# Kernel optimization log

Measured on AMD Instinct MI355X. Metric: run time of the kernel, lower is better.

## Reference

```python
import jax, jax.numpy as jnp
import numpy as np

EPS = 1e-12  # torch F.normalize default eps


def _l2norm(x):
    n = jnp.sqrt(jnp.sum(x * x, axis=-1, keepdims=True))
    return x / jnp.maximum(n, EPS)


def setup_inputs() -> dict:
    key = jax.random.key(0)
    ks = jax.random.split(key, 8)
    B, T, V = 4, 2048, 512
    C, H, NB = 512, 4, 64
    return {
        "x": jax.random.normal(ks[0], (B, T, V), dtype=jnp.float32),
        "basis": jax.random.normal(ks[1], (V, 2 * NB), dtype=jnp.float32),
        "shared_q_w": jax.random.normal(ks[2], (V, C), dtype=jnp.float32) * 0.02,
        "shared_k_w": jax.random.normal(ks[3], (V, C), dtype=jnp.float32) * 0.02,
        "v_coeffs": jax.random.normal(ks[4], (C, 2 * NB), dtype=jnp.float32) * 0.02,
        "o_coeffs": jax.random.normal(ks[5], (C, 2 * NB), dtype=jnp.float32) * 0.02,
        "decay_logits": jnp.linspace(1.0, 5.0, H, dtype=jnp.float32),
        "out_scale": jnp.float32(0.1),
    }


def reference(x, basis, shared_q_w, shared_k_w, v_coeffs, o_coeffs, decay_logits, out_scale):
    B, T, V = x.shape
    H = decay_logits.shape[0]
    C = shared_q_w.shape[1]
    D = C // H

    v_w = basis @ v_coeffs.T  # [V, C]
    o_w = basis @ o_coeffs.T  # [V, C]

    q = _l2norm(x @ shared_q_w)  # [B, T, C]
    k = _l2norm(x @ shared_k_w)
    v = x @ v_w

    # [B, H, T, D]
    q = q.reshape(B, T, H, D).transpose(0, 2, 1, 3)
    k = k.reshape(B, T, H, D).transpose(0, 2, 1, 3)
    v = v.reshape(B, T, H, D).transpose(0, 2, 1, 3)

    scores = jnp.einsum("bhqd,bhkd->bhqk", q, k)  # [B, H, T, T]

    decay = jax.nn.sigmoid(decay_logits)  # [H]
    pos = jnp.arange(T)
    diff = pos[None, :] - pos[:, None]  # diff[i, j] = j - i
    mask = (diff > 0).astype(scores.dtype)  # [T, T]
    expo = jnp.clip(diff.astype(jnp.float32) - 1.0, 0.0, None)  # [T, T]
    decay_w = (decay[:, None, None] ** expo[None]) * mask[None]  # [H, T, T]

    scores = scores * decay_w[None].astype(scores.dtype)
    retrieved = jnp.einsum("bhqk,bhkd->bhqd", scores, v)  # [B, H, T, D]
    retrieved = retrieved.transpose(0, 2, 1, 3).reshape(B, T, C)
    return retrieved @ o_w.T * out_scale  # [B, T, V]
```

## Files before the change

### kernel.cpp

```cpp
#include <hip/hip_runtime.h>
#include <hip/hip_bf16.h>

#define BB 4
#define TT 2048
#define VV 512
#define CC 512
#define HH 4
#define DD 128
#define NB2 128
#define NROWS (BB*TT)
#define QC 64
#define NCH (TT/QC)
#define SST 66
#define EPS 1e-12f

typedef __attribute__((ext_vector_type(8))) short bf16x8;
typedef __attribute__((ext_vector_type(4))) float f32x4;
typedef unsigned short u16;

__device__ __forceinline__ void gl_lds16(const void* g, void* l) {
    __builtin_amdgcn_global_load_lds(
        (const __attribute__((address_space(1))) unsigned int*)g,
        (__attribute__((address_space(3))) unsigned int*)l, 16, 0, 0);
}
__device__ __forceinline__ u16 f2bu(float x) {
    __hip_bfloat16 h = __float2bfloat16(x);
    return *reinterpret_cast<u16*>(&h);
}
__device__ __forceinline__ float bu2f(u16 u) {
    __hip_bfloat16 h = *reinterpret_cast<__hip_bfloat16*>(&u);
    return __bfloat162float(h);
}

#define PREP_CVT   4096
#define PREP_TR    512
#define PREP_CB    64
#define PREP_Z     16
__global__ __launch_bounds__(256) void prep_all(
    const float* __restrict__ x, const float* __restrict__ qw,
    const float* __restrict__ kw, const float* __restrict__ basis,
    const float* __restrict__ v_coeffs, const float* __restrict__ o_coeffs,
    const float* __restrict__ out_scale,
    u16* __restrict__ xb, u16* __restrict__ wq, u16* __restrict__ wk,
    u16* __restrict__ bab, u16* __restrict__ vcb, u16* __restrict__ ocb,
    float* __restrict__ norms)
{
    __shared__ float tile[32][33];
    const int bi = blockIdx.x, t = threadIdx.x;
    if (bi < PREP_CVT) {
        int i = bi * 256 + t;
        float4 v = ((const float4*)x)[i];
        u16 h[4] = {f2bu(v.x), f2bu(v.y), f2bu(v.z), f2bu(v.w)};
        ((uint2*)xb)[i] = *(uint2*)h;
    } else if (bi < PREP_CVT + PREP_TR) {
        int id = bi - PREP_CVT;
        const int z = id >> 8; id &= 255;
        const float* in = z ? kw : qw;
        u16* outT = z ? wk : wq;
        const int bx = (id & 15) * 32, by = (id >> 4) * 32;
        const int tx = t & 31, ty = t >> 5;
        #pragma unroll
        for (int r = 0; r < 32; r += 8)
            tile[ty + r][tx] = in[(size_t)(by + ty + r) * CC + bx + tx];
        __syncthreads();
        #pragma unroll
        for (int r = 0; r < 32; r += 8)
            outT[(size_t)(bx + ty + r) * VV + by + tx] = f2bu(tile[tx][ty + r]);
    } else if (bi < PREP_CVT + PREP_TR + 3 * PREP_CB) {
        int id = bi - PREP_CVT - PREP_TR;
        const int which = id / PREP_CB;
        int i = (id - which * PREP_CB) * 256 + t;
        const float* src = which == 0 ? basis : (which == 1 ? v_coeffs : o_coeffs);
        u16* dst = which == 0 ? bab : (which == 1 ? vcb : ocb);
        const float sc = which == 2 ? out_scale[0] : 1.f;
        float4 v = ((const float4*)src)[i];
        u16 h[4] = {f2bu(v.x * sc), f2bu(v.y * sc), f2bu(v.z * sc), f2bu(v.w * sc)};
        ((uint2*)dst)[i] = *(uint2*)h;
    } else {
        int idx = (bi - PREP_CVT - PREP_TR - 3 * PREP_CB) * 256 + t;
        ((float4*)norms)[idx] = make_float4(0.f, 0.f, 0.f, 0.f);
    }
}

template <bool BF16OUT, bool NORMS>
__device__ __forceinline__ void gemm_body(
    const u16* __restrict__ A, const u16* __restrict__ Bt,
    void* __restrict__ Cp, int M, int N, int K, int m0, int n0,
    u16* __restrict__ As, u16* __restrict__ Bs, float* __restrict__ normp)
{
    const int t = threadIdx.x;
    const int wave = t >> 6, lane = t & 63;
    const int qq = lane >> 4, l16 = lane & 15;
    const int wm = (wave >> 1) * 64, wn = (wave & 1) * 64;

    const int s0 = wave * 128 + lane, s1 = s0 + 64;
    const int r0_ = s0 >> 2, c0_ = ((s0 & 3) - (r0_ >> 1)) & 3;
    const int r1_ = s1 >> 2, c1_ = ((s1 & 3) - (r1_ >> 1)) & 3;
    const u16* ga0 = A  + (size_t)(m0 + r0_) * K + c0_ * 8;
    const u16* ga1 = A  + (size_t)(m0 + r1_) * K + c1_ * 8;
    const u16* gb0 = Bt + (size_t)(n0 + r0_) * K + c0_ * 8;
    const u16* gb1 = Bt + (size_t)(n0 + r1_) * K + c1_ * 8;
    const int lo0 = (wave * 128) * 8, lo1 = (wave * 128 + 64) * 8;

    gl_lds16(ga0, As + lo0);
    gl_lds16(ga1, As + lo1);
    gl_lds16(gb0, Bs + lo0);
    gl_lds16(gb1, Bs + lo1);

    f32x4 acc[4][4];
    #pragma unroll
    for (int i = 0; i < 4; ++i)
        #pragma unroll
        for (int j = 0; j < 4; ++j) acc[i][j] = (f32x4){0.f, 0.f, 0.f, 0.f};

    int ib = 0;
    for (int k0 = 0; k0 < K; k0 += 32, ib ^= 1) {
        __syncthreads();
        if (k0 + 32 < K) {
            const int off = (ib ^ 1) * 4096;
            gl_lds16(ga0 + k0 + 32, As + off + lo0);
            gl_lds16(ga1 + k0 + 32, As + off + lo1);
            gl_lds16(gb0 + k0 + 32, Bs + off + lo0);
            gl_lds16(gb1 + k0 + 32, Bs + off + lo1);
        }
        const u16* Ac = As + ib * 4096;
        const u16* Bc = Bs + ib * 4096;
        bf16x8 af[4], bfr[4];
        #pragma unroll
        for (int mt = 0; mt < 4; ++mt) {
            const int r = wm + mt * 16 + l16;
            af[mt] = *(const bf16x8*)&Ac[(r * 4 + ((qq + (r >> 1)) & 3)) * 8];
        }
        #pragma unroll
        for (int nt = 0; nt < 4; ++nt) {
            const int r = wn + nt * 16 + l16;
            bfr[nt] = *(const bf16x8*)&Bc[(r * 4 + ((qq + (r >> 1)) & 3)) * 8];
        }
        #pragma unroll
        for (int mt = 0; mt < 4; ++mt)
            #pragma unroll
            for (int nt = 0; nt < 4; ++nt)
                acc[mt][nt] = __builtin_amdgcn_mfma_f32_16x16x32_bf16(
                    af[mt], bfr[nt], acc[mt][nt], 0, 0, 0);
    }
    #pragma unroll
    for (int mt = 0; mt < 4; ++mt)
        #pragma unroll
        for (int r = 0; r < 4; ++r) {
            int grow = m0 + wm + mt * 16 + qq * 4 + r;
            #pragma unroll
            for (int nt = 0; nt < 4; ++nt) {
                int gcol = n0 + wn + nt * 16 + l16;
                if (BF16OUT)
                    ((u16*)Cp)[(size_t)grow * N + gcol] = f2bu(acc[mt][nt][r]);
                else
                    ((float*)Cp)[(size_t)grow * N + gcol] = acc[mt][nt][r];
            }
        }
    if (NORMS && normp) {
        #pragma unroll
        for (int mt = 0; mt < 4; ++mt)
            #pragma unroll
            for (int r = 0; r < 4; ++r) {
                float s = 0.f;
                #pragma unroll
                for (int nt = 0; nt < 4; ++nt) {
                    float v = acc[mt][nt][r];
                    s = fmaf(v, v, s);
                }
                s += __shfl_xor(s, 1, 64);
                s += __shfl_xor(s, 2, 64);
                s += __shfl_xor(s, 4, 64);
                s += __shfl_xor(s, 8, 64);
                if (l16 == 0)
                    atomicAdd(&normp[m0 + wm + mt * 16 + qq * 4 + r], s);
            }
    }
}

__global__ __launch_bounds__(256) void gemm_w(
    const u16* __restrict__ bab, const u16* __restrict__ vcb,
    const u16* __restrict__ ocb, u16* __restrict__ v_wT, u16* __restrict__ o_ws)
{
    __shared__ __align__(16) u16 As[8192];
    __shared__ __align__(16) u16 Bs[8192];
    const int sec = blockIdx.x >> 2;
    const u16* A  = sec ? bab : vcb;
    const u16* Bt = sec ? ocb : bab;
    u16* C = sec ? o_ws : v_wT;
    gemm_body<true, false>(A, Bt, C, 512, 512, NB2,
                           blockIdx.y * 128, (blockIdx.x & 3) * 128, As, Bs, nullptr);
}

__global__ __launch_bounds__(256) void gemm_qkv(
    const u16* __restrict__ xb, const u16* __restrict__ wcat,
    u16* __restrict__ qo, u16* __restrict__ ko, u16* __restrict__ vo,
    float* __restrict__ norms)
{
    __shared__ __align__(16) u16 As[8192];
    __shared__ __align__(16) u16 Bs[8192];
    const int sec = blockIdx.x >> 2;
    u16* outp = sec == 0 ? qo : (sec == 1 ? ko : vo);
    float* np = sec == 0 ? norms : (sec == 1 ? norms + NROWS : nullptr);
    gemm_body<true, true>(xb, wcat + (size_t)sec * VV * CC, outp,
                          NROWS, CC, VV, blockIdx.y * 128, (blockIdx.x & 3) * 128,
                          As, Bs, np);
}

__global__ __launch_bounds__(256) void gemm_out64(
    const u16* __restrict__ A, const u16* __restrict__ Bt, float* __restrict__ C)
{
    __shared__ __align__(16) u16 As[4096];
    __shared__ __align__(16) u16 Bs[8192];
    const int t = threadIdx.x;
    const int wave = t >> 6, lane = t & 63;
    const int qq = lane >> 4, l16 = lane & 15;
    const int m0 = blockIdx.y * 64, n0 = blockIdx.x * 128;
    const int wm = (wave >> 1) * 32, wn = (wave & 1) * 64;
    const int N = VV, K = CC;

    const int sA = wave * 64 + lane;
    const int rA = sA >> 2, cA = ((sA & 3) - (rA >> 1)) & 3;
    const int sB0 = wave * 128 + lane, sB1 = sB0 + 64;
    const int rB0 = sB0 >> 2, cB0 = ((sB0 & 3) - (rB0 >> 1)) & 3;
    const int rB1 = sB1 >> 2, cB1 = ((sB1 & 3) - (rB1 >> 1)) & 3;
    const u16* ga  = A  + (size_t)(m0 + rA) * K + cA * 8;
    const u16* gb0 = Bt + (size_t)(n0 + rB0) * K + cB0 * 8;
    const u16* gb1 = Bt + (size_t)(n0 + rB1) * K + cB1 * 8;
    const int loA = wave * 512, loB0 = wave * 1024, loB1 = wave * 1024 + 512;

    gl_lds16(ga, As + loA);
    gl_lds16(gb0, Bs + loB0);
    gl_lds16(gb1, Bs + loB1);

    f32x4 acc[2][4];
    #pragma unroll
    for (int i = 0; i < 2; ++i)
        #pragma unroll
        for (int j = 0; j < 4; ++j) acc[i][j] = (f32x4){0.f, 0.f, 0.f, 0.f};

    int ib = 0;
    for (int k0 = 0; k0 < K; k0 += 32, ib ^= 1) {
        __syncthreads();
        if (k0 + 32 < K) {
            gl_lds16(ga + k0 + 32,  As + (ib ^ 1) * 2048 + loA);
            gl_lds16(gb0 + k0 + 32, Bs + (ib ^ 1) * 4096 + loB0);
            gl_lds16(gb1 + k0 + 32, Bs + (ib ^ 1) * 4096 + loB1);
        }
        const u16* Ac = As + ib * 2048;
        const u16* Bc = Bs + ib * 4096;
        bf16x8 af[2], bfr[4];
        #pragma unroll
        for (int mt = 0; mt < 2; ++mt) {
            const int r = wm + mt * 16 + l16;
            af[mt] = *(const bf16x8*)&Ac[(r * 4 + ((qq + (r >> 1)) & 3)) * 8];
        }
        #pragma unroll
        for (int nt = 0; nt < 4; ++nt) {
            const int r = wn + nt * 16 + l16;
            bfr[nt] = *(const bf16x8*)&Bc[(r * 4 + ((qq + (r >> 1)) & 3)) * 8];
        }
        #pragma unroll
        for (int mt = 0; mt < 2; ++mt)
            #pragma unroll
            for (int nt = 0; nt < 4; ++nt)
                acc[mt][nt] = __builtin_amdgcn_mfma_f32_16x16x32_bf16(
                    af[mt], bfr[nt], acc[mt][nt], 0, 0, 0);
    }
    #pragma unroll
    for (int mt = 0; mt < 2; ++mt)
        #pragma unroll
        for (int r = 0; r < 4; ++r) {
            int grow = m0 + wm + mt * 16 + qq * 4 + r;
            #pragma unroll
            for (int nt = 0; nt < 4; ++nt)
                C[(size_t)grow * N + n0 + wn + nt * 16 + l16] = acc[mt][nt][r];
        }
}

__global__ __launch_bounds__(256) void state_local(
    const u16* __restrict__ kb, const u16* __restrict__ vb,
    const float* __restrict__ norms_k, const float* __restrict__ dlog,
    u16* __restrict__ statesb)
{
    __shared__ __align__(16) u16 vT[DD][SST];
    __shared__ __align__(16) u16 kT[DD][SST];
    const int c = blockIdx.x, bh = blockIdx.y;
    const int b = bh >> 2, h = bh & 3;
    const float lam = 1.f / (1.f + __expf(-dlog[h]));
    const float l2lam = log2f(lam);
    const int t = threadIdx.x;
    const int row0 = b * TT + c * QC;
    const size_t gbase = (size_t)row0 * CC + h * DD;

    {
        const int j2 = t & 31, d0 = (t >> 5) * 16;
        const int jj0 = 2 * j2, jj1 = jj0 + 1;
        const float w0 = exp2f((float)jj0 * l2lam);
        const float w1 = exp2f((float)jj1 * l2lam);
        const float rk0 = 1.f / fmaxf(sqrtf(norms_k[row0 + jj0]), EPS);
        const float rk1 = 1.f / fmaxf(sqrtf(norms_k[row0 + jj1]), EPS);
        u16 k0a[16], k1a[16], v0a[16], v1a[16];
        const u16* k0p = kb + gbase + (size_t)jj0 * CC + d0;
        const u16* k1p = kb + gbase + (size_t)jj1 * CC + d0;
        const u16* v0p = vb + gbase + (size_t)jj0 * CC + d0;
        const u16* v1p = vb + gbase + (size_t)jj1 * CC + d0;
        *(uint4*)&k0a[0] = *(const uint4*)k0p; *(uint4*)&k0a[8] = *(const uint4*)(k0p + 8);
        *(uint4*)&k1a[0] = *(const uint4*)k1p; *(uint4*)&k1a[8] = *(const uint4*)(k1p + 8);
        *(uint4*)&v0a[0] = *(const uint4*)v0p; *(uint4*)&v0a[8] = *(const uint4*)(v0p + 8);
        *(uint4*)&v1a[0] = *(const uint4*)v1p; *(uint4*)&v1a[8] = *(const uint4*)(v1p + 8);
        #pragma unroll
        for (int i = 0; i < 16; ++i) {
            unsigned int kw = (unsigned int)f2bu(bu2f(k0a[i]) * rk0)
                            | ((unsigned int)f2bu(bu2f(k1a[i]) * rk1) << 16);
            *(unsigned int*)&kT[d0 + i][jj0] = kw;
            unsigned int vw = (unsigned int)f2bu(bu2f(v0a[i]) * w0)
                            | ((unsigned int)f2bu(bu2f(v1a[i]) * w1) << 16);
            *(unsigned int*)&vT[d0 + i][jj0] = vw;
        }
    }
    __syncthreads();

    const int wave = t >> 6, lane = t & 63;
    const int quad = lane >> 4, l16 = lane & 15;
    f32x4 acc[2][8];
    #pragma unroll
    for (int i = 0; i < 2; ++i)
        #pragma unroll
        for (int j = 0; j < 8; ++j) acc[i][j] = (f32x4){0.f, 0.f, 0.f, 0.f};

    #pragma unroll
    for (int s = 0; s < 2; ++s) {
        bf16x8 af[2];
        #pragma unroll
        for (int mt = 0; mt < 2; ++mt)
            af[mt] = *(const bf16x8*)&vT[wave * 32 + mt * 16 + l16][s * 32 + quad * 8];
        #pragma unroll
        for (int nt = 0; nt < 8; ++nt) {
            bf16x8 bk = *(const bf16x8*)&kT[nt * 16 + l16][s * 32 + quad * 8];
            #pragma unroll
            for (int mt = 0; mt < 2; ++mt)
                acc[mt][nt] = __builtin_amdgcn_mfma_f32_16x16x32_bf16(
                    af[mt], bk, acc[mt][nt], 0, 0, 0);
        }
    }
    u16* so = statesb + ((size_t)(bh * NCH + c) << 14);
    #pragma unroll
    for (int mt = 0; mt < 2; ++mt)
        #pragma unroll
        for (int rr = 0; rr < 4; ++rr) {
            const int d = wave * 32 + mt * 16 + quad * 4 + rr;
            #pragma unroll
            for (int nt = 0; nt < 8; ++nt)
                so[(size_t)d * DD + nt * 16 + l16] = f2bu(acc[mt][nt][rr]);
        }
}

__global__ __launch_bounds__(256) void state_combine(
    const float* __restrict__ dlog, u16* __restrict__ statesb)
{
    const int bh = blockIdx.x >> 3, part = blockIdx.x & 7;
    const int h = bh & 3;
    const float lam = 1.f / (1.f + __expf(-dlog[h]));
    const float lamQ = exp2f((float)QC * log2f(lam));
    const int t = threadIdx.x;
    float run[8] = {};
    uint4* pbase = (uint4*)(statesb + ((size_t)(bh * NCH) << 14)) + part * 256 + t;
    uint4 cur = pbase[(size_t)(NCH - 1) * 2048];
    for (int c = NCH - 1; c >= 0; --c) {
        uint4 nxt = cur;
        if (c) nxt = pbase[(size_t)(c - 1) * 2048];
        u16* hb = (u16*)&cur;
        uint4 outw;
        u16* ho = (u16*)&outw;
        #pragma unroll
        for (int i = 0; i < 8; ++i) {
            float tmp = bu2f(hb[i]);
            ho[i] = f2bu(run[i]);
            run[i] = fmaf(lamQ, run[i], tmp);
        }
        pbase[(size_t)c * 2048] = outw;
        cur = nxt;
    }
}

__global__ __launch_bounds__(256) void attention_fused(
    const u16* __restrict__ qb, const u16* __restrict__ kb,
    const u16* __restrict__ vb, const u16* __restrict__ statesb,
    const float* __restrict__ norms, const float* __restrict__ dlog,
    u16* __restrict__ retb)
{
    __shared__ __align__(16) u16 qks[2 * QC * DD];
    __shared__ __align__(16) u16 vsT[DD][SST];
    __shared__ __align__(16) u16 ss[QC][SST];
    __shared__ float rql[QC], rkl[QC];

    const int c = blockIdx.x, bh = blockIdx.y;
    const int b = bh >> 2, h = bh & 3;
    const float lam = 1.f / (1.f + __expf(-dlog[h]));
    const float l2lam = log2f(lam);
    const int t = threadIdx.x;
    const int row0 = b * TT + c * QC;
    const size_t base = (size_t)row0 * CC + h * DD;

    const int wave = t >> 6, lane = t & 63;
    const int quad = lane >> 4, l16 = lane & 15;
    const int r0 = wave * 16;

    {
        const int lrow = lane >> 4, cch = lane & 15;
        #pragma unroll
        for (int u = 0; u < 4; ++u) {
            const int R = wave * 16 + u * 4;
            const int gr = R + lrow;
            const int cq = (cch - gr) & 15;
            gl_lds16(qb + base + (size_t)gr * CC + cq * 8, &qks[R * DD]);
            gl_lds16(kb + base + (size_t)gr * CC + cq * 8, &qks[(QC + R) * DD]);
        }
    }
    if (t < QC)            rql[t]      = 1.f / fmaxf(sqrtf(norms[row0 + t]), EPS);
    else if (t < 2 * QC)   rkl[t - QC] = 1.f / fmaxf(sqrtf(norms[NROWS + row0 + t - QC]), EPS);
    {
        const int j2 = t & 31, d0 = (t >> 5) * 16;
        const u16* v0 = vb + base + (size_t)(2 * j2) * CC + d0;
        const u16* v1 = v0 + CC;
        uint4 a0 = *(const uint4*)v0;
        uint4 a1 = *(const uint4*)(v0 + 8);
        uint4 b0 = *(const uint4*)v1;
        uint4 b1 = *(const uint4*)(v1 + 8);
        const u16* ap0 = (const u16*)&a0; const u16* ap1 = (const u16*)&a1;
        const u16* bp0 = (const u16*)&b0; const u16* bp1 = (const u16*)&b1;
        #pragma unroll
        for (int i = 0; i < 8; ++i) {
            *(unsigned int*)&vsT[d0 + i][2 * j2] =
                (unsigned int)ap0[i] | ((unsigned int)bp0[i] << 16);
            *(unsigned int*)&vsT[d0 + 8 + i][2 * j2] =
                (unsigned int)ap1[i] | ((unsigned int)bp1[i] << 16);
        }
    }
    __syncthreads();

    bf16x8 aq[4];
    #pragma unroll
    for (int kq = 0; kq < 4; ++kq) {
        const int r = r0 + l16;
        aq[kq] = *(const bf16x8*)&qks[r * DD + ((kq * 4 + quad + r) & 15) * 8];
    }

    f32x4 accs[4];
    #pragma unroll
    for (int nt = 0; nt < 4; ++nt) accs[nt] = (f32x4){0.f, 0.f, 0.f, 0.f};
    #pragma unroll
    for (int nt = 0; nt < 4; ++nt)
        #pragma unroll
        for (int kq = 0; kq < 4; ++kq) {
            const int rk_ = nt * 16 + l16;
            bf16x8 bk = *(const bf16x8*)&qks[(QC + rk_) * DD + ((kq * 4 + quad + rk_) & 15) * 8];
            accs[nt] = __builtin_amdgcn_mfma_f32_16x16x32_bf16(aq[kq], bk, accs[nt], 0, 0, 0);
        }

    #pragma unroll
    for (int nt = 0; nt < 4; ++nt) {
        const int j = nt * 16 + l16;
        const float rkj = rkl[j];
        #pragma unroll
        for (int rr = 0; rr < 4; ++rr) {
            const int i = r0 + quad * 4 + rr;
            const int di = j - i;
            float p = (di > 0) ? accs[nt][rr] * exp2f((float)(di - 1) * l2lam) * rkj : 0.f;
            ss[i][j] = f2bu(p);
        }
    }
    __syncthreads();

    const u16* sb = statesb + ((size_t)(bh * NCH + c) << 14);
    {
        const int drow = lane >> 4, cch = lane & 15;
        #pragma unroll
        for (int u = 0; u < 8; ++u) {
            const int D = wave * 32 + u * 4;
            const int gd = D + drow;
            const int cq = (cch - gd) & 15;
            gl_lds16(sb + (size_t)gd * DD + cq * 8, &qks[D * DD]);
        }
    }
    bf16x8 ap[2];
    #pragma unroll
    for (int kj = 0; kj < 2; ++kj)
        ap[kj] = *(const bf16x8*)&ss[r0 + l16][kj * 32 + quad * 8];
    f32x4 accd[8];
    #pragma unroll
    for (int nt = 0; nt < 8; ++nt) accd[nt] = (f32x4){0.f, 0.f, 0.f, 0.f};
    #pragma unroll
    for (int nt = 0; nt < 8; ++nt)
        #pragma unroll
        for (int kj = 0; kj < 2; ++kj) {
            bf16x8 bv = *(const bf16x8*)&vsT[nt * 16 + l16][kj * 32 + quad * 8];
            accd[nt] = __builtin_amdgcn_mfma_f32_16x16x32_bf16(ap[kj], bv, accd[nt], 0, 0, 0);
        }
    __syncthreads();

    f32x4 accc[8];
    #pragma unroll
    for (int nt = 0; nt < 8; ++nt) accc[nt] = (f32x4){0.f, 0.f, 0.f, 0.f};
    #pragma unroll
    for (int nt = 0; nt < 8; ++nt)
        #pragma unroll
        for (int kq = 0; kq < 4; ++kq) {
            const int d = nt * 16 + l16;
            bf16x8 bs_ = *(const bf16x8*)&qks[d * DD + ((kq * 4 + quad + d) & 15) * 8];
            accc[nt] = __builtin_amdgcn_mfma_f32_16x16x32_bf16(aq[kq], bs_, accc[nt], 0, 0, 0);
        }

    u16* rb = retb + (size_t)row0 * CC + h * DD;
    #pragma unroll
    for (int rr = 0; rr < 4; ++rr) {
        const int ii = r0 + quad * 4 + rr;
        const float wrow = exp2f((float)(QC - 1 - ii) * l2lam);
        const float rq = rql[ii];
        #pragma unroll
        for (int nt = 0; nt < 8; ++nt) {
            float val = (accd[nt][rr] + wrow * accc[nt][rr]) * rq;
            rb[(size_t)ii * CC + nt * 16 + l16] = f2bu(val);
        }
    }
}

extern "C" void kernel_launch(void* const* d_in, const int* in_sizes, int n_in,
                              void* d_out, int out_size, void* d_ws, size_t ws_size,
                              hipStream_t stream) {
    const float* x         = (const float*)d_in[0];
    const float* basis     = (const float*)d_in[1];
    const float* qw        = (const float*)d_in[2];
    const float* kw        = (const float*)d_in[3];
    const float* v_coeffs  = (const float*)d_in[4];
    const float* o_coeffs  = (const float*)d_in[5];
    const float* dlog      = (const float*)d_in[6];
    const float* out_scale = (const float*)d_in[7];
    float* out             = (float*)d_out;

    u16* p = (u16*)d_ws;
    u16* qb      = p;
    u16* kb      = qb + (size_t)NROWS * CC;
    u16* vb      = kb + (size_t)NROWS * CC;
    u16* statesb = vb + (size_t)NROWS * CC;
    u16* xb      = statesb + (size_t)BB * HH * NCH * DD * DD;
    u16* retb    = xb;
    u16* wcat    = xb + (size_t)NROWS * CC;
    u16* o_ws    = wcat + 3 * (size_t)VV * CC;
    float* norms = (float*)(o_ws + (size_t)VV * CC);
    u16* bab     = (u16*)(norms + 2 * NROWS);
    u16* vcb     = bab + (size_t)VV * NB2;
    u16* ocb     = vcb + (size_t)VV * NB2;

    prep_all<<<PREP_CVT + PREP_TR + 3 * PREP_CB + PREP_Z, 256, 0, stream>>>(
        x, qw, kw, basis, v_coeffs, o_coeffs, out_scale,
        xb, wcat, wcat + (size_t)VV * CC, bab, vcb, ocb, norms);
    gemm_w<<<dim3(8, 4), 256, 0, stream>>>(bab, vcb, ocb,
                                           wcat + 2 * (size_t)VV * CC, o_ws);
    gemm_qkv<<<dim3(12, NROWS / 128), 256, 0, stream>>>(xb, wcat, qb, kb, vb, norms);
    state_local  <<<dim3(NCH, BB * HH), 256, 0, stream>>>(kb, vb, norms + NROWS,
                                                          dlog, statesb);
    state_combine<<<BB * HH * 8, 256, 0, stream>>>(dlog, statesb);
    attention_fused<<<dim3(NCH, BB * HH), 256, 0, stream>>>(qb, kb, vb, statesb,
                                                            norms, dlog, retb);
    gemm_out64<<<dim3(VV / 128, NROWS / 64), 256, 0, stream>>>(retb, o_ws, out);
}
```

Measured before the change: 168.9 us.

## Fuse Q/K/V projection GEMMs into one kernel sharing the X tile

Replaces the 12-column-block QKV GEMM grid with a kernel in which each block computes the Q, K and V outputs for the same 128x128 tile. The X tile is loaded once per K-step and reused across all three weight matrices. This cuts redundant global loads of X and shrinks the grid from 12x64 to 4x64 blocks. In exchange each thread holds three times as many accumulators, which raises register pressure (launch bounds set to one block per SM). The 256 blocks may also underfill the GPU's compute units.

```diff
diff --git a/kernel.cpp b/kernel.cpp
--- a/kernel.cpp
+++ b/kernel.cpp
@@ -82,11 +82,10 @@
     }
 }
 
-template <bool BF16OUT, bool NORMS>
 __device__ __forceinline__ void gemm_body(
     const u16* __restrict__ A, const u16* __restrict__ Bt,
-    void* __restrict__ Cp, int M, int N, int K, int m0, int n0,
-    u16* __restrict__ As, u16* __restrict__ Bs, float* __restrict__ normp)
+    u16* __restrict__ Cp, int N, int K, int m0, int n0,
+    u16* __restrict__ As, u16* __restrict__ Bs)
 {
     const int t = threadIdx.x;
     const int wave = t >> 6, lane = t & 63;
@@ -149,33 +148,9 @@
         for (int r = 0; r < 4; ++r) {
             int grow = m0 + wm + mt * 16 + qq * 4 + r;
             #pragma unroll
-            for (int nt = 0; nt < 4; ++nt) {
-                int gcol = n0 + wn + nt * 16 + l16;
-                if (BF16OUT)
-                    ((u16*)Cp)[(size_t)grow * N + gcol] = f2bu(acc[mt][nt][r]);
-                else
-                    ((float*)Cp)[(size_t)grow * N + gcol] = acc[mt][nt][r];
-            }
-        }
-    if (NORMS && normp) {
-        #pragma unroll
-        for (int mt = 0; mt < 4; ++mt)
-            #pragma unroll
-            for (int r = 0; r < 4; ++r) {
-                float s = 0.f;
-                #pragma unroll
-                for (int nt = 0; nt < 4; ++nt) {
-                    float v = acc[mt][nt][r];
-                    s = fmaf(v, v, s);
-                }
-                s += __shfl_xor(s, 1, 64);
-                s += __shfl_xor(s, 2, 64);
-                s += __shfl_xor(s, 4, 64);
-                s += __shfl_xor(s, 8, 64);
-                if (l16 == 0)
-                    atomicAdd(&normp[m0 + wm + mt * 16 + qq * 4 + r], s);
-            }
-    }
+            for (int nt = 0; nt < 4; ++nt)
+                Cp[(size_t)grow * N + n0 + wn + nt * 16 + l16] = f2bu(acc[mt][nt][r]);
+        }
 }
 
 __global__ __launch_bounds__(256) void gemm_w(
@@ -188,23 +163,124 @@
     const u16* A  = sec ? bab : vcb;
     const u16* Bt = sec ? ocb : bab;
     u16* C = sec ? o_ws : v_wT;
-    gemm_body<true, false>(A, Bt, C, 512, 512, NB2,
-                           blockIdx.y * 128, (blockIdx.x & 3) * 128, As, Bs, nullptr);
-}
-
-__global__ __launch_bounds__(256) void gemm_qkv(
+    gemm_body(A, Bt, C, 512, NB2, blockIdx.y * 128, (blockIdx.x & 3) * 128, As, Bs);
+}
+
+__global__ __launch_bounds__(256, 1) void gemm_qkv_fused(
     const u16* __restrict__ xb, const u16* __restrict__ wcat,
     u16* __restrict__ qo, u16* __restrict__ ko, u16* __restrict__ vo,
     float* __restrict__ norms)
 {
-    __shared__ __align__(16) u16 As[8192];
-    __shared__ __align__(16) u16 Bs[8192];
-    const int sec = blockIdx.x >> 2;
-    u16* outp = sec == 0 ? qo : (sec == 1 ? ko : vo);
-    float* np = sec == 0 ? norms : (sec == 1 ? norms + NROWS : nullptr);
-    gemm_body<true, true>(xb, wcat + (size_t)sec * VV * CC, outp,
-                          NROWS, CC, VV, blockIdx.y * 128, (blockIdx.x & 3) * 128,
-                          As, Bs, np);
+    __shared__ __align__(16) u16 As[2 * 4096];
+    __shared__ __align__(16) u16 Bs[3 * 2 * 4096];
+    const int t = threadIdx.x;
+    const int wave = t >> 6, lane = t & 63;
+    const int qq = lane >> 4, l16 = lane & 15;
+    const int m0 = blockIdx.y * 128, n0 = blockIdx.x * 128;
+    const int wm = (wave >> 1) * 64, wn = (wave & 1) * 64;
+    const int K = VV;
+
+    const int s0 = wave * 128 + lane, s1 = s0 + 64;
+    const int r0_ = s0 >> 2, c0_ = ((s0 & 3) - (r0_ >> 1)) & 3;
+    const int r1_ = s1 >> 2, c1_ = ((s1 & 3) - (r1_ >> 1)) & 3;
+    const u16* ga0 = xb + (size_t)(m0 + r0_) * K + c0_ * 8;
+    const u16* ga1 = xb + (size_t)(m0 + r1_) * K + c1_ * 8;
+    const u16* gb0[3];
+    const u16* gb1[3];
+    #pragma unroll
+    for (int sec = 0; sec < 3; ++sec) {
+        gb0[sec] = wcat + (size_t)sec * VV * CC + (size_t)(n0 + r0_) * K + c0_ * 8;
+        gb1[sec] = wcat + (size_t)sec * VV * CC + (size_t)(n0 + r1_) * K + c1_ * 8;
+    }
+    const int lo0 = (wave * 128) * 8, lo1 = lo0 + 512;
+
+    gl_lds16(ga0, As + lo0);
+    gl_lds16(ga1, As + lo1);
+    #pragma unroll
+    for (int sec = 0; sec < 3; ++sec) {
+        gl_lds16(gb0[sec], Bs + sec * 8192 + lo0);
+        gl_lds16(gb1[sec], Bs + sec * 8192 + lo1);
+    }
+
+    f32x4 acc[3][4][4];
+    #pragma unroll
+    for (int s = 0; s < 3; ++s)
+        #pragma unroll
+        for (int i = 0; i < 4; ++i)
+            #pragma unroll
+            for (int j = 0; j < 4; ++j) acc[s][i][j] = (f32x4){0.f, 0.f, 0.f, 0.f};
+
+    int ib = 0;
+    for (int k0 = 0; k0 < K; k0 += 32, ib ^= 1) {
+        __syncthreads();
+        if (k0 + 32 < K) {
+            const int off = (ib ^ 1) * 4096;
+            gl_lds16(ga0 + k0 + 32, As + off + lo0);
+            gl_lds16(ga1 + k0 + 32, As + off + lo1);
+            #pragma unroll
+            for (int sec = 0; sec < 3; ++sec) {
+                gl_lds16(gb0[sec] + k0 + 32, Bs + sec * 8192 + off + lo0);
+                gl_lds16(gb1[sec] + k0 + 32, Bs + sec * 8192 + off + lo1);
+            }
+        }
+        const u16* Ac = As + ib * 4096;
+        bf16x8 af[4];
+        #pragma unroll
+        for (int mt = 0; mt < 4; ++mt) {
+            const int r = wm + mt * 16 + l16;
+            af[mt] = *(const bf16x8*)&Ac[(r * 4 + ((qq + (r >> 1)) & 3)) * 8];
+        }
+        #pragma unroll
+        for (int sec = 0; sec < 3; ++sec) {
+            const u16* Bc = Bs + sec * 8192 + ib * 4096;
+            bf16x8 bfr[4];
+            #pragma unroll
+            for (int nt = 0; nt < 4; ++nt) {
+                const int r = wn + nt * 16 + l16;
+                bfr[nt] = *(const bf16x8*)&Bc[(r * 4 + ((qq + (r >> 1)) & 3)) * 8];
+            }
+            #pragma unroll
+            for (int mt = 0; mt < 4; ++mt)
+                #pragma unroll
+                for (int nt = 0; nt < 4; ++nt)
+                    acc[sec][mt][nt] = __builtin_amdgcn_mfma_f32_16x16x32_bf16(
+                        af[mt], bfr[nt], acc[sec][mt][nt], 0, 0, 0);
+        }
+    }
+    #pragma unroll
+    for (int sec = 0; sec < 3; ++sec) {
+        u16* outp = sec == 0 ? qo : (sec == 1 ? ko : vo);
+        #pragma unroll
+        for (int mt = 0; mt < 4; ++mt)
+            #pragma unroll
+            for (int r = 0; r < 4; ++r) {
+                int grow = m0 + wm + mt * 16 + qq * 4 + r;
+                #pragma unroll
+                for (int nt = 0; nt < 4; ++nt)
+                    outp[(size_t)grow * CC + n0 + wn + nt * 16 + l16] =
+                        f2bu(acc[sec][mt][nt][r]);
+            }
+        if (sec < 2) {
+            float* np = sec == 0 ? norms : norms + NROWS;
+            #pragma unroll
+            for (int mt = 0; mt < 4; ++mt)
+                #pragma unroll
+                for (int r = 0; r < 4; ++r) {
+                    float s = 0.f;
+                    #pragma unroll
+                    for (int nt = 0; nt < 4; ++nt) {
+                        float v = acc[sec][mt][nt][r];
+                        s = fmaf(v, v, s);
+                    }
+                    s += __shfl_xor(s, 1, 64);
+                    s += __shfl_xor(s, 2, 64);
+                    s += __shfl_xor(s, 4, 64);
+                    s += __shfl_xor(s, 8, 64);
+                    if (l16 == 0)
+                        atomicAdd(&np[m0 + wm + mt * 16 + qq * 4 + r], s);
+                }
+        }
+    }
 }
 
 __global__ __launch_bounds__(256) void gemm_out64(
@@ -558,7 +634,8 @@
         xb, wcat, wcat + (size_t)VV * CC, bab, vcb, ocb, norms);
     gemm_w<<<dim3(8, 4), 256, 0, stream>>>(bab, vcb, ocb,
                                            wcat + 2 * (size_t)VV * CC, o_ws);
-    gemm_qkv<<<dim3(12, NROWS / 128), 256, 0, stream>>>(xb, wcat, qb, kb, vb, norms);
+    gemm_qkv_fused<<<dim3(4, NROWS / 128), 256, 0, stream>>>(xb, wcat, qb, kb, vb,
+                                                             norms);
     state_local  <<<dim3(NCH, BB * HH), 256, 0, stream>>>(kb, vb, norms + NROWS,
                                                           dlog, statesb);
     state_combine<<<BB * HH * 8, 256, 0, stream>>>(dlog, statesb);
```

Result: no change. 168.6 us (-0.2%).
